# Optimization experiments

Hardware: AMD Instinct MI355X
Metric: run time of the kernel (lower is better)

## Reference

```python
import jax, jax.numpy as jnp
import numpy as np

B, T, U, D, V = 8, 256, 64, 640, 1024  # batch, enc frames, target len, per-stream dim, vocab


def setup_inputs() -> dict:
    key = jax.random.key(0)
    k1, k2, k3, k4 = jax.random.split(key, 4)
    return {
        "source_encodings": jax.random.normal(k1, (B, T, D), dtype=jnp.float32),
        "source_lengths": jnp.full((B,), T, dtype=jnp.int32),  # full lengths -> static packed shape
        "target_encodings": jax.random.normal(k2, (B, U, D), dtype=jnp.float32),
        "target_lengths": jnp.full((B,), U, dtype=jnp.int32),
        "W": jax.random.normal(k3, (V, 2 * D), dtype=jnp.float32) / np.sqrt(2 * D).astype(np.float32),
        "b": jax.random.normal(k4, (V,), dtype=jnp.float32) * 0.01,
    }


def reference(source_encodings, source_lengths, target_encodings, target_lengths, W, b):
    # Per-batch broadcast-concat over the (T, U) joint lattice, then flatten rows.
    # With full lengths this equals the torch per-sample loop (same row order).
    enc = jnp.broadcast_to(source_encodings[:, :, None, :], (B, T, U, D))   # [B,T,U,D]
    pred = jnp.broadcast_to(target_encodings[:, None, :, :], (B, T, U, D))  # [B,T,U,D]
    joint_input = jnp.concatenate([enc, pred], axis=-1).reshape(B * T * U, 2 * D)
    # joiner: dropout(p=0 -> identity) -> ReLU -> Linear
    activation_out = jax.nn.relu(joint_input)
    joint_output = activation_out @ W.T + b  # [B*T*U, V]
    return joint_output, source_lengths, target_lengths
```

## Files before the change

kernel.cpp:

```cpp
#include <hip/hip_runtime.h>


#define BM 64
#define BN 64
#define BK 16
#define TPAD 4

__global__ __launch_bounds__(256) void gemm_relu_kernel(
    const float* __restrict__ enc,
    const float* __restrict__ pred,
    const float* __restrict__ W,
    const float* __restrict__ bias,
    float* __restrict__ E,
    float* __restrict__ P)
{
    __shared__ float As[BK][BM + TPAD];
    __shared__ float Bs[BK][BN + TPAD];

    const int tid  = threadIdx.x;
    const int row0 = blockIdx.y * BM;
    const int col0 = blockIdx.x * BN;

    const bool isE = row0 < 2048;
    const float* A = isE ? (enc + (size_t)row0 * 640)
                         : (pred + (size_t)(row0 - 2048) * 640);
    float* outp    = isE ? (E + (size_t)row0 * 1024)
                         : (P + (size_t)(row0 - 2048) * 1024);
    const int woff = isE ? 0 : 640;

    const int lm = tid >> 2;
    const int lk = (tid & 3) * 4;

    const int tx = tid & 15;
    const int ty = tid >> 4;

    float acc[4][4];
    #pragma unroll
    for (int i = 0; i < 4; ++i)
        #pragma unroll
        for (int j = 0; j < 4; ++j) acc[i][j] = 0.f;

    for (int k0 = 0; k0 < 640; k0 += BK) {
        float4 a4 = *(const float4*)(A + (size_t)lm * 640 + k0 + lk);
        float4 b4 = *(const float4*)(W + (size_t)(col0 + lm) * 1280 + woff + k0 + lk);
        As[lk + 0][lm] = fmaxf(a4.x, 0.f);
        As[lk + 1][lm] = fmaxf(a4.y, 0.f);
        As[lk + 2][lm] = fmaxf(a4.z, 0.f);
        As[lk + 3][lm] = fmaxf(a4.w, 0.f);
        Bs[lk + 0][lm] = b4.x;
        Bs[lk + 1][lm] = b4.y;
        Bs[lk + 2][lm] = b4.z;
        Bs[lk + 3][lm] = b4.w;
        __syncthreads();

        #pragma unroll
        for (int k = 0; k < BK; ++k) {
            float4 av = *(const float4*)&As[k][ty * 4];
            float4 bv = *(const float4*)&Bs[k][tx * 4];
            float ar[4] = {av.x, av.y, av.z, av.w};
            float br[4] = {bv.x, bv.y, bv.z, bv.w};
            #pragma unroll
            for (int i = 0; i < 4; ++i)
                #pragma unroll
                for (int j = 0; j < 4; ++j)
                    acc[i][j] = fmaf(ar[i], br[j], acc[i][j]);
        }
        __syncthreads();
    }

    float4 bb = make_float4(0.f, 0.f, 0.f, 0.f);
    if (isE) bb = *(const float4*)(bias + col0 + tx * 4);

    #pragma unroll
    for (int i = 0; i < 4; ++i) {
        float4 o;
        o.x = acc[i][0] + bb.x;
        o.y = acc[i][1] + bb.y;
        o.z = acc[i][2] + bb.z;
        o.w = acc[i][3] + bb.w;
        *(float4*)(outp + (size_t)(ty * 4 + i) * 1024 + col0 + tx * 4) = o;
    }
}

__global__ __launch_bounds__(256) void bcast_add_kernel(
    const float* __restrict__ E,
    const float* __restrict__ P,
    float* __restrict__ out)
{
    const int bt  = blockIdx.x;
    const int b   = bt >> 8;
    const int tid = threadIdx.x;

    const float4 e4 = ((const float4*)(E + (size_t)bt * 1024))[tid];
    const float4* Pb = (const float4*)(P + (size_t)b * 64 * 1024);
    float4* ob = (float4*)(out + (size_t)bt * 64 * 1024);

    #pragma unroll 4
    for (int u = 0; u < 64; ++u) {
        float4 p4 = Pb[u * 256 + tid];
        float4 o;
        o.x = e4.x + p4.x;
        o.y = e4.y + p4.y;
        o.z = e4.z + p4.z;
        o.w = e4.w + p4.w;
        ob[u * 256 + tid] = o;
    }
}

__global__ void lengths_kernel(const int* __restrict__ sl,
                               const int* __restrict__ tl,
                               float* __restrict__ out_tail)
{
    const int i = threadIdx.x;
    if (i < 8) {
        out_tail[i]     = (float)sl[i];
        out_tail[8 + i] = (float)tl[i];
    }
}

extern "C" void kernel_launch(void* const* d_in, const int* in_sizes, int n_in,
                              void* d_out, int out_size, void* d_ws, size_t ws_size,
                              hipStream_t stream) {
    const float* enc  = (const float*)d_in[0];
    const int*   sl   = (const int*)d_in[1];
    const float* pred = (const float*)d_in[2];
    const int*   tl   = (const int*)d_in[3];
    const float* W    = (const float*)d_in[4];
    const float* bias = (const float*)d_in[5];

    float* out = (float*)d_out;
    float* E = (float*)d_ws;
    float* P = E + 2048 * 1024;

    dim3 g1(1024 / BN, 2560 / BM);
    gemm_relu_kernel<<<g1, 256, 0, stream>>>(enc, pred, W, bias, E, P);

    bcast_add_kernel<<<2048, 256, 0, stream>>>(E, P, out);

    lengths_kernel<<<1, 64, 0, stream>>>(sl, tl, out + (size_t)131072 * 1024);
}
```

Before: 614.7 us.

## Fuse encoder GEMM with broadcast-add and use nontemporal output stores

The encoder-side projection GEMM is now computed inside the broadcast-add kernel, so the E intermediate is no longer written to and re-read from workspace. Each block computes a 16-frame by 256-vocab tile of E in registers, then streams the sum with the precomputed P rows to the output using nontemporal stores. The predictor GEMM stays a separate small kernel. The fused kernel has few threads (128) and a larger per-thread tile, so occupancy and GEMM efficiency may drop, but the dominant cost is the roughly 512 MB output write.

```diff
diff --git a/kernel.cpp b/kernel.cpp
--- a/kernel.cpp
+++ b/kernel.cpp
@@ -1,36 +1,27 @@
 #include <hip/hip_runtime.h>
 
 
-#define BM 64
-#define BN 64
-#define BK 16
-#define TPAD 4
+typedef float floatx4 __attribute__((ext_vector_type(4)));
 
-__global__ __launch_bounds__(256) void gemm_relu_kernel(
-    const float* __restrict__ enc,
+#define PBM 64
+#define PBN 64
+#define PBK 16
+#define PPAD 4
+
+__global__ __launch_bounds__(256) void p_gemm_kernel(
     const float* __restrict__ pred,
     const float* __restrict__ W,
-    const float* __restrict__ bias,
-    float* __restrict__ E,
     float* __restrict__ P)
 {
-    __shared__ float As[BK][BM + TPAD];
-    __shared__ float Bs[BK][BN + TPAD];
+    __shared__ float As[PBK][PBM + PPAD];
+    __shared__ float Bs[PBK][PBN + PPAD];
 
     const int tid  = threadIdx.x;
-    const int row0 = blockIdx.y * BM;
-    const int col0 = blockIdx.x * BN;
-
-    const bool isE = row0 < 2048;
-    const float* A = isE ? (enc + (size_t)row0 * 640)
-                         : (pred + (size_t)(row0 - 2048) * 640);
-    float* outp    = isE ? (E + (size_t)row0 * 1024)
-                         : (P + (size_t)(row0 - 2048) * 1024);
-    const int woff = isE ? 0 : 640;
+    const int row0 = blockIdx.y * PBM;
+    const int col0 = blockIdx.x * PBN;
 
     const int lm = tid >> 2;
     const int lk = (tid & 3) * 4;
-
     const int tx = tid & 15;
     const int ty = tid >> 4;
 
@@ -40,9 +31,9 @@
         #pragma unroll
         for (int j = 0; j < 4; ++j) acc[i][j] = 0.f;
 
-    for (int k0 = 0; k0 < 640; k0 += BK) {
-        float4 a4 = *(const float4*)(A + (size_t)lm * 640 + k0 + lk);
-        float4 b4 = *(const float4*)(W + (size_t)(col0 + lm) * 1280 + woff + k0 + lk);
+    for (int k0 = 0; k0 < 640; k0 += PBK) {
+        float4 a4 = *(const float4*)(pred + (size_t)(row0 + lm) * 640 + k0 + lk);
+        float4 b4 = *(const float4*)(W + (size_t)(col0 + lm) * 1280 + 640 + k0 + lk);
         As[lk + 0][lm] = fmaxf(a4.x, 0.f);
         As[lk + 1][lm] = fmaxf(a4.y, 0.f);
         As[lk + 2][lm] = fmaxf(a4.z, 0.f);
@@ -54,7 +45,7 @@
         __syncthreads();
 
         #pragma unroll
-        for (int k = 0; k < BK; ++k) {
+        for (int k = 0; k < PBK; ++k) {
             float4 av = *(const float4*)&As[k][ty * 4];
             float4 bv = *(const float4*)&Bs[k][tx * 4];
             float ar[4] = {av.x, av.y, av.z, av.w};
@@ -68,42 +59,111 @@
         __syncthreads();
     }
 
-    float4 bb = make_float4(0.f, 0.f, 0.f, 0.f);
-    if (isE) bb = *(const float4*)(bias + col0 + tx * 4);
-
     #pragma unroll
     for (int i = 0; i < 4; ++i) {
         float4 o;
-        o.x = acc[i][0] + bb.x;
-        o.y = acc[i][1] + bb.y;
-        o.z = acc[i][2] + bb.z;
-        o.w = acc[i][3] + bb.w;
-        *(float4*)(outp + (size_t)(ty * 4 + i) * 1024 + col0 + tx * 4) = o;
+        o.x = acc[i][0]; o.y = acc[i][1]; o.z = acc[i][2]; o.w = acc[i][3];
+        *(float4*)(P + (size_t)(row0 + ty * 4 + i) * 1024 + col0 + tx * 4) = o;
     }
 }
 
-__global__ __launch_bounds__(256) void bcast_add_kernel(
-    const float* __restrict__ E,
+
+#define TT 16
+#define VT 256
+#define KB 16
+
+__global__ __launch_bounds__(128) void e_fused_kernel(
+    const float* __restrict__ enc,
+    const float* __restrict__ W,
+    const float* __restrict__ bias,
     const float* __restrict__ P,
     float* __restrict__ out)
 {
-    const int bt  = blockIdx.x;
-    const int b   = bt >> 8;
-    const int tid = threadIdx.x;
+    __shared__ float As[KB][TT];
+    __shared__ float Ws[KB][VT];
 
-    const float4 e4 = ((const float4*)(E + (size_t)bt * 1024))[tid];
-    const float4* Pb = (const float4*)(P + (size_t)b * 64 * 1024);
-    float4* ob = (float4*)(out + (size_t)bt * 64 * 1024);
+    const int t   = threadIdx.x;
+    const int vt  = blockIdx.x;
+    const int tt  = blockIdx.y;
+    const int bt0 = tt * TT;
+    const int v0  = vt * VT;
+    const int b   = bt0 >> 8;
+
+    const int w  = t >> 6;
+    const int l  = t & 63;
+    const int w8 = w * 8;
+    const int l4 = l * 4;
+
+    float acc[8][4];
+    #pragma unroll
+    for (int i = 0; i < 8; ++i)
+        #pragma unroll
+        for (int j = 0; j < 4; ++j) acc[i][j] = 0.f;
+
+    for (int k0 = 0; k0 < 640; k0 += KB) {
+        if (t < 64) {
+            const int row = t & 15;
+            const int kq  = t >> 4;
+            float4 a4 = *(const float4*)(enc + (size_t)(bt0 + row) * 640 + k0 + kq * 4);
+            As[kq * 4 + 0][row] = fmaxf(a4.x, 0.f);
+            As[kq * 4 + 1][row] = fmaxf(a4.y, 0.f);
+            As[kq * 4 + 2][row] = fmaxf(a4.z, 0.f);
+            As[kq * 4 + 3][row] = fmaxf(a4.w, 0.f);
+        }
+        #pragma unroll
+        for (int p = 0; p < 2; ++p) {
+            const int vv = t * 2 + p;
+            const float* wp = W + (size_t)(v0 + vv) * 1280 + k0;
+            float4 q0 = ((const float4*)wp)[0];
+            float4 q1 = ((const float4*)wp)[1];
+            float4 q2 = ((const float4*)wp)[2];
+            float4 q3 = ((const float4*)wp)[3];
+            Ws[ 0][vv] = q0.x; Ws[ 1][vv] = q0.y; Ws[ 2][vv] = q0.z; Ws[ 3][vv] = q0.w;
+            Ws[ 4][vv] = q1.x; Ws[ 5][vv] = q1.y; Ws[ 6][vv] = q1.z; Ws[ 7][vv] = q1.w;
+            Ws[ 8][vv] = q2.x; Ws[ 9][vv] = q2.y; Ws[10][vv] = q2.z; Ws[11][vv] = q2.w;
+            Ws[12][vv] = q3.x; Ws[13][vv] = q3.y; Ws[14][vv] = q3.z; Ws[15][vv] = q3.w;
+        }
+        __syncthreads();
+
+        #pragma unroll
+        for (int k = 0; k < KB; ++k) {
+            float4 a0 = *(const float4*)&As[k][w8];
+            float4 a1 = *(const float4*)&As[k][w8 + 4];
+            float4 bv = *(const float4*)&Ws[k][l4];
+            float ar[8] = {a0.x, a0.y, a0.z, a0.w, a1.x, a1.y, a1.z, a1.w};
+            float br[4] = {bv.x, bv.y, bv.z, bv.w};
+            #pragma unroll
+            for (int i = 0; i < 8; ++i)
+                #pragma unroll
+                for (int j = 0; j < 4; ++j)
+                    acc[i][j] = fmaf(ar[i], br[j], acc[i][j]);
+        }
+        __syncthreads();
+    }
+
+    {
+        float4 bb = *(const float4*)(bias + v0 + l4);
+        #pragma unroll
+        for (int i = 0; i < 8; ++i) {
+            acc[i][0] += bb.x; acc[i][1] += bb.y; acc[i][2] += bb.z; acc[i][3] += bb.w;
+        }
+    }
+
+    const float* Pb = P + (size_t)b * 65536 + v0 + l4;
+    float* ob = out + (size_t)(bt0 + w8) * 65536 + v0 + l4;
 
     #pragma unroll 4
     for (int u = 0; u < 64; ++u) {
-        float4 p4 = Pb[u * 256 + tid];
-        float4 o;
-        o.x = e4.x + p4.x;
-        o.y = e4.y + p4.y;
-        o.z = e4.z + p4.z;
-        o.w = e4.w + p4.w;
-        ob[u * 256 + tid] = o;
+        float4 p4 = *(const float4*)(Pb + (size_t)u * 1024);
+        #pragma unroll
+        for (int i = 0; i < 8; ++i) {
+            floatx4 o;
+            o.x = acc[i][0] + p4.x;
+            o.y = acc[i][1] + p4.y;
+            o.z = acc[i][2] + p4.z;
+            o.w = acc[i][3] + p4.w;
+            __builtin_nontemporal_store(o, (floatx4*)(ob + (size_t)i * 65536 + (size_t)u * 1024));
+        }
     }
 }
 
@@ -129,13 +189,11 @@
     const float* bias = (const float*)d_in[5];
 
     float* out = (float*)d_out;
-    float* E = (float*)d_ws;
-    float* P = E + 2048 * 1024;
+    float* P   = (float*)d_ws;
 
-    dim3 g1(1024 / BN, 2560 / BM);
-    gemm_relu_kernel<<<g1, 256, 0, stream>>>(enc, pred, W, bias, E, P);
+    p_gemm_kernel<<<dim3(16, 8), 256, 0, stream>>>(pred, W, P);
 
-    bcast_add_kernel<<<2048, 256, 0, stream>>>(E, P, out);
+    e_fused_kernel<<<dim3(4, 128), 128, 0, stream>>>(enc, W, bias, P, out);
 
     lengths_kernel<<<1, 64, 0, stream>>>(sl, tl, out + (size_t)131072 * 1024);
 }
```

After: 668.1 us. 1.09x slower.
